# Kernel optimization log

Hardware: AMD Instinct MI355X
Metric: run time of the kernel (lower is better)

Reference implementation:

```python
import jax, jax.numpy as jnp
import numpy as np


def setup_inputs() -> dict:
    key = jax.random.key(0)
    ks = jax.random.split(key, 5)
    B, T, I, H, O = 256, 2048, 256, 256, 16
    x = jax.random.normal(ks[0], (B, T, I), dtype=jnp.float32)
    W_ih = jax.random.normal(ks[1], (I, H), dtype=jnp.float32) * 0.05
    W_hh = jax.random.normal(ks[2], (H, H), dtype=jnp.float32) * 0.05
    b_h = jnp.zeros((H,), dtype=jnp.float32)
    fc_w = jax.random.normal(ks[3], (O, H), dtype=jnp.float32) * 0.05
    fc_b = jnp.zeros((O,), dtype=jnp.float32)
    return {"x": x, "W_ih": W_ih, "W_hh": W_hh, "b_h": b_h, "fc_w": fc_w, "fc_b": fc_b}


def reference(x, W_ih, W_hh, b_h, fc_w, fc_b):
    # x: [B, T, I]. Precompute input projections for all timesteps in one GEMM,
    # then scan the strictly sequential hidden-state recurrence.
    B, T, I = x.shape
    H = W_hh.shape[0]
    xp = jnp.einsum('bti,ih->tbh', x, W_ih) + b_h  # [T, B, H]

    def step(h, xt):
        h = jnp.tanh(xt + h @ W_hh)
        return h, None

    h0 = jnp.zeros((B, H), dtype=x.dtype)
    h_final, _ = jax.lax.scan(step, h0, xp)
    return h_final @ fc_w.T + fc_b  # [B, O]
```

## Files before the change

### kernel.cpp

```cpp
#include <hip/hip_runtime.h>
#include <hip/hip_bf16.h>


typedef _Float16 f16;
typedef _Float16 h8_t __attribute__((ext_vector_type(8)));
typedef _Float16 h2_t __attribute__((ext_vector_type(2)));
typedef float    f4_t __attribute__((ext_vector_type(4)));

__device__ __forceinline__ float fdot2u(unsigned w, unsigned h, float c) {
  return __builtin_amdgcn_fdot2(__builtin_bit_cast(h2_t, w),
                                __builtin_bit_cast(h2_t, h), c, false);
}
__device__ __forceinline__ unsigned pkrtz(float a, float b) {
  return __builtin_bit_cast(unsigned, __builtin_amdgcn_cvt_pkrtz(a, b));
}

__global__ __launch_bounds__(256) void prep_kernel(const float* __restrict__ Wih,
                                                   const float* __restrict__ Whh,
                                                   uint4* __restrict__ Wfrag,
                                                   uint4* __restrict__ Wc2) {
  int idx = blockIdx.x * 256 + threadIdx.x;
  int e = idx & 8191;
  int gi = e >> 8;
  int lg = e & 255;
  int w = lg >> 6, l = lg & 63;
  unsigned r[4];
  if (idx < 8192) {
    int nt = gi >> 3, ks = gi & 7;
    int n = w * 64 + nt * 16 + (l & 15);
    int k0 = ks * 32 + (l >> 4) * 8;
#pragma unroll
    for (int c = 0; c < 4; ++c)
      r[c] = pkrtz(Wih[(k0 + 2 * c) * 256 + n], Wih[(k0 + 2 * c + 1) * 256 + n]);
    Wfrag[gi * 256 + lg] = make_uint4(r[0], r[1], r[2], r[3]);
  } else {
    int oi = gi >> 3, q2 = gi & 7;
    int j = l + 64 * oi;
    int kb = 64 * w + 8 * q2;
#pragma unroll
    for (int c = 0; c < 4; ++c)
      r[c] = pkrtz(Whh[(kb + 2 * c) * 256 + j], Whh[(kb + 2 * c + 1) * 256 + j]);
    Wc2[gi * 256 + lg] = make_uint4(r[0], r[1], r[2], r[3]);
  }
}

__global__ __launch_bounds__(256, 2) void gemm_kernel(const float* __restrict__ x,
                                                      const uint4* __restrict__ Wfrag,
                                                      f16* __restrict__ xp,
                                                      int t0, int CT, int tpc) {
  __shared__ f16 As[64][264];
  int tid = threadIdx.x;
  int wave = tid >> 6, l = tid & 63, l15 = l & 15, q = l >> 4;

  uint4 bf[4][8];
#pragma unroll
  for (int nt = 0; nt < 4; ++nt)
#pragma unroll
    for (int ks = 0; ks < 8; ++ks)
      bf[nt][ks] = Wfrag[(nt * 8 + ks) * 256 + tid];

  int blk = blockIdx.x;
  int b = blk / tpc, tt = blk - b * tpc;
  int tl0 = tt * 64;

  const uint4* xsrc = (const uint4*)(x + ((size_t)b * 2048 + t0 + tl0) * 256);
#pragma unroll
  for (int i = 0; i < 16; ++i) {
    int fi = i * 256 + tid;
    float4 f = __builtin_bit_cast(float4, xsrc[fi]);
    int row = fi >> 6;
    int k = (fi & 63) * 4;
    uint2 pv; pv.x = pkrtz(f.x, f.y); pv.y = pkrtz(f.z, f.w);
    *(uint2*)&As[row][k] = pv;
  }
  __syncthreads();

  f4_t acc[4][4];
#pragma unroll
  for (int mt = 0; mt < 4; ++mt)
#pragma unroll
    for (int nt = 0; nt < 4; ++nt) acc[mt][nt] = (f4_t){0.f, 0.f, 0.f, 0.f};

  for (int mt = 0; mt < 4; ++mt) {
    uint4 af[8];
#pragma unroll
    for (int ks = 0; ks < 8; ++ks)
      af[ks] = *(const uint4*)&As[mt * 16 + l15][ks * 32 + q * 8];
#pragma unroll
    for (int ks = 0; ks < 8; ++ks) {
      h8_t a = __builtin_bit_cast(h8_t, af[ks]);
#pragma unroll
      for (int nt = 0; nt < 4; ++nt)
        acc[mt][nt] = __builtin_amdgcn_mfma_f32_16x16x32_f16(
            a, __builtin_bit_cast(h8_t, bf[nt][ks]), acc[mt][nt], 0, 0, 0);
    }
  }

  f16* xpo = xp + (size_t)b * CT * 256;
#pragma unroll
  for (int mt = 0; mt < 4; ++mt)
#pragma unroll
    for (int nt = 0; nt < 4; ++nt) {
      int n = wave * 64 + nt * 16 + l15;
#pragma unroll
      for (int r = 0; r < 4; ++r)
        xpo[(size_t)(tl0 + mt * 16 + q * 4 + r) * 256 + n] = (f16)acc[mt][nt][r];
    }
}

__global__ __launch_bounds__(256, 1) void rnn_kernel(const f16* __restrict__ xp,
                                                     const uint4* __restrict__ Wc2,
                                                     const float* __restrict__ b_h,
                                                     const float* __restrict__ fc_w,
                                                     const float* __restrict__ fc_b,
                                                     float* __restrict__ hstate,
                                                     float* __restrict__ out,
                                                     int t0, int CT) {
  __shared__ f16 hbuf[2][256];
  __shared__ float prt[4][256];
  __shared__ float hf[256];
  __shared__ float prt2[16][16];

  int b = blockIdx.x, tid = threadIdx.x;
  int w = tid >> 6, l = tid & 63;

  uint4 wv[32];
#pragma unroll
  for (int g = 0; g < 32; ++g) wv[g] = Wc2[g * 256 + tid];

  float hcur = (t0 == 0) ? 0.0f : hstate[b * 256 + tid];
  hbuf[0][tid] = (f16)hcur;
  float bhv = b_h[tid];

  const f16* xpb = xp + (size_t)b * CT * 256 + tid;
  float xv = (float)xpb[0];
  float xn = (float)xpb[256];
  __syncthreads();

  for (int tt = 0; tt < CT; ++tt) {
    int pf = (tt + 2 < CT) ? tt + 2 : CT - 1;
    f16 xf = xpb[(size_t)pf * 256];

    const uint4* hb = (const uint4*)&hbuf[tt & 1][w * 64];
    uint4 hh[8];
#pragma unroll
    for (int q2 = 0; q2 < 8; ++q2) hh[q2] = hb[q2];

    float s[4];
#pragma unroll
    for (int oi = 0; oi < 4; ++oi) {
      float a0 = 0.f, a1 = 0.f;
#pragma unroll
      for (int q2 = 0; q2 < 8; ++q2) {
        uint4 wq = wv[oi * 8 + q2];
        a0 = fdot2u(wq.x, hh[q2].x, a0);
        a1 = fdot2u(wq.y, hh[q2].y, a1);
        a0 = fdot2u(wq.z, hh[q2].z, a0);
        a1 = fdot2u(wq.w, hh[q2].w, a1);
      }
      s[oi] = a0 + a1;
    }
#pragma unroll
    for (int oi = 0; oi < 4; ++oi) prt[w][l + 64 * oi] = s[oi];
    __syncthreads();

    float z = prt[0][tid] + prt[1][tid] + prt[2][tid] + prt[3][tid] + xv + bhv;
    float e = __expf(2.0f * z);
    hcur = 1.0f - 2.0f * __builtin_amdgcn_rcpf(e + 1.0f);
    hbuf[(tt + 1) & 1][tid] = (f16)hcur;
    xv = xn;
    xn = (float)xf;
    __syncthreads();
  }

  hstate[b * 256 + tid] = hcur;

  if (t0 + CT == 2048) {
    hf[tid] = hcur;
    __syncthreads();
    int o = tid >> 4, s2 = tid & 15;
    const float* fw = fc_w + o * 256 + s2 * 16;
    float p = 0.f;
#pragma unroll
    for (int i = 0; i < 16; ++i) p += hf[s2 * 16 + i] * fw[i];
    prt2[o][s2] = p;
    __syncthreads();
    if (tid < 16) {
      float r = fc_b[tid];
#pragma unroll
      for (int s3 = 0; s3 < 16; ++s3) r += prt2[tid][s3];
      out[b * 16 + tid] = r;
    }
  }
}

extern "C" void kernel_launch(void* const* d_in, const int* in_sizes, int n_in,
                              void* d_out, int out_size, void* d_ws, size_t ws_size,
                              hipStream_t stream) {
  const float* x   = (const float*)d_in[0];
  const float* Wih = (const float*)d_in[1];
  const float* Whh = (const float*)d_in[2];
  const float* bh  = (const float*)d_in[3];
  const float* fcw = (const float*)d_in[4];
  const float* fcb = (const float*)d_in[5];
  float* out = (float*)d_out;

  char* ws = (char*)d_ws;
  uint4* Wfrag  = (uint4*)ws;
  uint4* Wc2    = (uint4*)(ws + (128 << 10));
  float* hstate = (float*)(ws + (256 << 10));
  f16*   xpb    = (f16*)(ws + (512 << 10));

  size_t avail = (ws_size > (size_t)(512 << 10)) ? ws_size - (size_t)(512 << 10) : 0;
  int CT = 2048;
  while (CT > 64 && (size_t)CT * 131072 > avail) CT >>= 1;
  int tpc = CT >> 6;

  prep_kernel<<<64, 256, 0, stream>>>(Wih, Whh, Wfrag, Wc2);
  for (int t0 = 0; t0 < 2048; t0 += CT) {
    gemm_kernel<<<256 * tpc, 256, 0, stream>>>(x, Wfrag, xpb, t0, CT, tpc);
    rnn_kernel<<<256, 256, 0, stream>>>(xpb, Wc2, bh, fcw, fcb, hstate, out, t0, CT);
  }
}
```

Before: 1.969 ms.

## Drop a per-step barrier in RNN loop and amortize GEMM weight loads

The recurrence loop now uses double-buffered partial-sum storage and a single hidden-state buffer. Each wave reads only the hidden entries its own lanes wrote, so one of the two block barriers per timestep can be removed. The input-projection prefetch is deepened to four steps. The GEMM kernel now processes several 64-row tiles per block, so the register-resident weight fragments are loaded once per several tiles, with empty asm constraints pinning them in registers. The risk is that correctness depends on the wave-local ownership of hidden entries, plus higher register pressure.

```diff
diff --git a/kernel.cpp b/kernel.cpp
--- a/kernel.cpp
+++ b/kernel.cpp
@@ -13,6 +13,9 @@
 }
 __device__ __forceinline__ unsigned pkrtz(float a, float b) {
   return __builtin_bit_cast(unsigned, __builtin_amdgcn_cvt_pkrtz(a, b));
+}
+__device__ __forceinline__ void pin4(uint4& v) {
+  asm volatile("" : "+v"(v.x), "+v"(v.y), "+v"(v.z), "+v"(v.w));
 }
 
 __global__ __launch_bounds__(256) void prep_kernel(const float* __restrict__ Wih,
@@ -47,7 +50,8 @@
 __global__ __launch_bounds__(256, 2) void gemm_kernel(const float* __restrict__ x,
                                                       const uint4* __restrict__ Wfrag,
                                                       f16* __restrict__ xp,
-                                                      int t0, int CT, int tpc) {
+                                                      int t0, int CT,
+                                                      int tpb, int bpb) {
   __shared__ f16 As[64][264];
   int tid = threadIdx.x;
   int wave = tid >> 6, l = tid & 63, l15 = l & 15, q = l >> 4;
@@ -58,54 +62,55 @@
 #pragma unroll
     for (int ks = 0; ks < 8; ++ks)
       bf[nt][ks] = Wfrag[(nt * 8 + ks) * 256 + tid];
-
-  int blk = blockIdx.x;
-  int b = blk / tpc, tt = blk - b * tpc;
-  int tl0 = tt * 64;
-
-  const uint4* xsrc = (const uint4*)(x + ((size_t)b * 2048 + t0 + tl0) * 256);
-#pragma unroll
-  for (int i = 0; i < 16; ++i) {
-    int fi = i * 256 + tid;
-    float4 f = __builtin_bit_cast(float4, xsrc[fi]);
-    int row = fi >> 6;
-    int k = (fi & 63) * 4;
-    uint2 pv; pv.x = pkrtz(f.x, f.y); pv.y = pkrtz(f.z, f.w);
-    *(uint2*)&As[row][k] = pv;
-  }
-  __syncthreads();
-
-  f4_t acc[4][4];
-#pragma unroll
-  for (int mt = 0; mt < 4; ++mt)
-#pragma unroll
-    for (int nt = 0; nt < 4; ++nt) acc[mt][nt] = (f4_t){0.f, 0.f, 0.f, 0.f};
-
-  for (int mt = 0; mt < 4; ++mt) {
-    uint4 af[8];
-#pragma unroll
-    for (int ks = 0; ks < 8; ++ks)
-      af[ks] = *(const uint4*)&As[mt * 16 + l15][ks * 32 + q * 8];
-#pragma unroll
-    for (int ks = 0; ks < 8; ++ks) {
-      h8_t a = __builtin_bit_cast(h8_t, af[ks]);
-#pragma unroll
-      for (int nt = 0; nt < 4; ++nt)
-        acc[mt][nt] = __builtin_amdgcn_mfma_f32_16x16x32_f16(
-            a, __builtin_bit_cast(h8_t, bf[nt][ks]), acc[mt][nt], 0, 0, 0);
-    }
-  }
-
+#pragma unroll
+  for (int nt = 0; nt < 4; ++nt)
+#pragma unroll
+    for (int ks = 0; ks < 8; ++ks) pin4(bf[nt][ks]);
+
+  int b = blockIdx.x / bpb;
+  int tb = blockIdx.x - b * bpb;
   f16* xpo = xp + (size_t)b * CT * 256;
-#pragma unroll
-  for (int mt = 0; mt < 4; ++mt)
-#pragma unroll
-    for (int nt = 0; nt < 4; ++nt) {
-      int n = wave * 64 + nt * 16 + l15;
-#pragma unroll
-      for (int r = 0; r < 4; ++r)
-        xpo[(size_t)(tl0 + mt * 16 + q * 4 + r) * 256 + n] = (f16)acc[mt][nt][r];
-    }
+
+  for (int sub = 0; sub < tpb; ++sub) {
+    int tl0 = (tb * tpb + sub) * 64;
+    const uint4* xsrc = (const uint4*)(x + ((size_t)b * 2048 + t0 + tl0) * 256);
+    __syncthreads();
+#pragma unroll 4
+    for (int i = 0; i < 16; ++i) {
+      int fi = i * 256 + tid;
+      float4 f = __builtin_bit_cast(float4, xsrc[fi]);
+      int row = fi >> 6;
+      int k = (fi & 63) * 4;
+      uint2 pv; pv.x = pkrtz(f.x, f.y); pv.y = pkrtz(f.z, f.w);
+      *(uint2*)&As[row][k] = pv;
+    }
+    __syncthreads();
+
+    for (int mt = 0; mt < 4; ++mt) {
+      uint4 af[8];
+#pragma unroll
+      for (int ks = 0; ks < 8; ++ks)
+        af[ks] = *(const uint4*)&As[mt * 16 + l15][ks * 32 + q * 8];
+      f4_t acc[4];
+#pragma unroll
+      for (int nt = 0; nt < 4; ++nt) acc[nt] = (f4_t){0.f, 0.f, 0.f, 0.f};
+#pragma unroll
+      for (int ks = 0; ks < 8; ++ks) {
+        h8_t a = __builtin_bit_cast(h8_t, af[ks]);
+#pragma unroll
+        for (int nt = 0; nt < 4; ++nt)
+          acc[nt] = __builtin_amdgcn_mfma_f32_16x16x32_f16(
+              a, __builtin_bit_cast(h8_t, bf[nt][ks]), acc[nt], 0, 0, 0);
+      }
+#pragma unroll
+      for (int nt = 0; nt < 4; ++nt) {
+        int n = wave * 64 + nt * 16 + l15;
+#pragma unroll
+        for (int r = 0; r < 4; ++r)
+          xpo[(size_t)(tl0 + mt * 16 + q * 4 + r) * 256 + n] = (f16)acc[nt][r];
+      }
+    }
+  }
 }
 
 __global__ __launch_bounds__(256, 1) void rnn_kernel(const f16* __restrict__ xp,
@@ -116,8 +121,8 @@
                                                      float* __restrict__ hstate,
                                                      float* __restrict__ out,
                                                      int t0, int CT) {
-  __shared__ f16 hbuf[2][256];
-  __shared__ float prt[4][256];
+  __shared__ f16 hbuf[256];
+  __shared__ float prt[2][4][256];
   __shared__ float hf[256];
   __shared__ float prt2[16][16];
 
@@ -127,21 +132,27 @@
   uint4 wv[32];
 #pragma unroll
   for (int g = 0; g < 32; ++g) wv[g] = Wc2[g * 256 + tid];
+#pragma unroll
+  for (int g = 0; g < 32; ++g) pin4(wv[g]);
 
   float hcur = (t0 == 0) ? 0.0f : hstate[b * 256 + tid];
-  hbuf[0][tid] = (f16)hcur;
+  hbuf[tid] = (f16)hcur;
   float bhv = b_h[tid];
 
   const f16* xpb = xp + (size_t)b * CT * 256 + tid;
-  float xv = (float)xpb[0];
-  float xn = (float)xpb[256];
-  __syncthreads();
+  f16 xq[4];
+#pragma unroll
+  for (int i = 0; i < 4; ++i) {
+    int p = (i < CT) ? i : CT - 1;
+    xq[i] = xpb[(size_t)p * 256];
+  }
 
   for (int tt = 0; tt < CT; ++tt) {
-    int pf = (tt + 2 < CT) ? tt + 2 : CT - 1;
-    f16 xf = xpb[(size_t)pf * 256];
-
-    const uint4* hb = (const uint4*)&hbuf[tt & 1][w * 64];
+    float xv = (float)xq[tt & 3];
+    int pf = (tt + 4 < CT) ? tt + 4 : CT - 1;
+    xq[tt & 3] = xpb[(size_t)pf * 256];
+
+    const uint4* hb = (const uint4*)&hbuf[w * 64];
     uint4 hh[8];
 #pragma unroll
     for (int q2 = 0; q2 < 8; ++q2) hh[q2] = hb[q2];
@@ -160,17 +171,16 @@
       }
       s[oi] = a0 + a1;
     }
-#pragma unroll
-    for (int oi = 0; oi < 4; ++oi) prt[w][l + 64 * oi] = s[oi];
-    __syncthreads();
-
-    float z = prt[0][tid] + prt[1][tid] + prt[2][tid] + prt[3][tid] + xv + bhv;
+    float* pw = prt[tt & 1][w];
+#pragma unroll
+    for (int oi = 0; oi < 4; ++oi) pw[l + 64 * oi] = s[oi];
+    __syncthreads();
+
+    const float (*pr)[256] = prt[tt & 1];
+    float z = pr[0][tid] + pr[1][tid] + pr[2][tid] + pr[3][tid] + xv + bhv;
     float e = __expf(2.0f * z);
     hcur = 1.0f - 2.0f * __builtin_amdgcn_rcpf(e + 1.0f);
-    hbuf[(tt + 1) & 1][tid] = (f16)hcur;
-    xv = xn;
-    xn = (float)xf;
-    __syncthreads();
+    hbuf[tid] = (f16)hcur;
   }
 
   hstate[b * 256 + tid] = hcur;
@@ -214,11 +224,13 @@
   size_t avail = (ws_size > (size_t)(512 << 10)) ? ws_size - (size_t)(512 << 10) : 0;
   int CT = 2048;
   while (CT > 64 && (size_t)CT * 131072 > avail) CT >>= 1;
-  int tpc = CT >> 6;
+
+  int tpb = (CT >= 256) ? 4 : (CT >> 6);
+  int bpb = CT / (64 * tpb);
 
   prep_kernel<<<64, 256, 0, stream>>>(Wih, Whh, Wfrag, Wc2);
   for (int t0 = 0; t0 < 2048; t0 += CT) {
-    gemm_kernel<<<256 * tpc, 256, 0, stream>>>(x, Wfrag, xpb, t0, CT, tpc);
+    gemm_kernel<<<256 * bpb, 256, 0, stream>>>(x, Wfrag, xpb, t0, CT, tpb, bpb);
     rnn_kernel<<<256, 256, 0, stream>>>(xpb, Wc2, bh, fcw, fcb, hstate, out, t0, CT);
   }
 }
```

Result: slower. 2.302 ms (+16.9%).
